# Kernel tuning notes

Hardware: AMD Instinct MI355X
Metric: run time of the kernel (lower is better)

The kernel has to match this reference:

```python
import jax, jax.numpy as jnp
import numpy as np

B, M, FIN, OUT, K = 64, 512, 128, 128, 2
SLOPE = 0.01  # F.leaky_relu default negative_slope


def setup_inputs() -> dict:
    key = jax.random.key(0)
    k0, k1, k2, k3 = jax.random.split(key, 4)
    x = jax.random.normal(k0, (B, M, FIN), jnp.float32)
    La = jax.random.normal(k1, (B, M, M), jnp.float32)
    weight = jax.random.normal(k2, (FIN * K, OUT), jnp.float32) * np.sqrt(2.0 / (FIN * K + OUT))
    bias = jnp.zeros((OUT,), jnp.float32)
    M_L = jax.random.normal(k3, (FIN, FIN), jnp.float32) * np.sqrt(2.0 / FIN)
    return {"x": x, "La": La, "weight": weight, "bias": bias, "M_L": M_L}


def _leaky(v):
    return jnp.where(v >= 0, v, SLOPE * v)


def _per_mol(xm, Lm, weight, bias, M_L):
    # xm: [M, FIN], Lm: [M, M]
    # compute_laplacian: pairwise Euclidean distances of x @ M_L via gram trick
    xw = xm @ M_L                                   # [M, FIN]
    sq = jnp.sum(xw * xw, axis=-1)                  # [M]
    d2 = sq[:, None] + sq[None, :] - 2.0 * (xw @ xw.T)
    dist = jnp.sqrt(jnp.maximum(d2, 1e-12))         # safe sqrt (diag is 0)
    W = jnp.exp(-dist)                              # [M, M]
    d = W.sum(axis=1) + 1e-7
    dis = 1.0 / jnp.sqrt(d)
    L = jnp.eye(M, dtype=xm.dtype) - dis[:, None] * W * dis[None, :]
    # clip_by_average_norm(clip_norm=1)
    avg_norm = jnp.linalg.norm(L) / (M * M)
    factor = jnp.minimum(1.0 / (avg_norm + 1e-6), 1.0)
    res_L = _leaky(L * factor)
    L_all = res_L + Lm
    # Chebyshev recursion (K terms)
    xs = [xm]
    if K > 1:
        xs.append(L_all @ xm)
    for _ in range(2, K):
        xs.append(2.0 * (L_all @ xs[-1]) - xs[-2])
    xk = jnp.stack(xs, axis=0)                      # [K, M, FIN]
    xk = jnp.transpose(xk, (1, 2, 0)).reshape(M, K * FIN)  # matches permute(1,2,0).view
    out = _leaky(xk @ weight + bias)                # activation 'relu' maps to leaky_relu
    return out, res_L, W


def reference(x, La, weight, bias, M_L):
    out, L_upd, W_upd = jax.vmap(lambda xm, Lm: _per_mol(xm, Lm, weight, bias, M_L))(x, La)
    return out, L_upd, W_upd
```

## Files before the change

kernel.cpp:

```cpp
#include <hip/hip_runtime.h>


#define BB 64
#define MM 512
#define FINC 128
#define OUTC 128

typedef short bf16x8 __attribute__((ext_vector_type(8)));
typedef float f32x4 __attribute__((ext_vector_type(4)));

__device__ __forceinline__ float leaky_(float v) { return v >= 0.0f ? v : 0.01f * v; }
__device__ __forceinline__ unsigned short f2bf(float f) {
    unsigned int u = __float_as_uint(f);
    return (unsigned short)((u + 0x7FFF + ((u >> 16) & 1)) >> 16);
}

__global__ __launch_bounds__(256) void k_xw(const float* __restrict__ x,
                                            const float* __restrict__ ml,
                                            unsigned short* __restrict__ xwb,
                                            float* __restrict__ sq,
                                            unsigned short* __restrict__ xTb) {
    const int b = blockIdx.y, i0 = blockIdx.x * 64;
    const int tid = threadIdx.x, ty4 = (tid >> 4) * 4, tx4 = (tid & 15) * 4;
    __shared__ float a_t[64][129];
    __shared__ float b_t[64][129];
    __shared__ float red[64][17];

    const float* xb = x + ((size_t)b * MM + i0) * FINC;
#pragma unroll
    for (int q = 0; q < 8; ++q) {
        int idx4 = tid + q * 256;
        int r = idx4 >> 5, k4 = (idx4 & 31) * 4;
        float4 v = *(const float4*)(xb + r * FINC + k4);
        a_t[r][k4 + 0] = v.x; a_t[r][k4 + 1] = v.y;
        a_t[r][k4 + 2] = v.z; a_t[r][k4 + 3] = v.w;
    }

    float acc[4][8];
#pragma unroll
    for (int m = 0; m < 4; ++m)
#pragma unroll
        for (int n = 0; n < 8; ++n) acc[m][n] = 0.0f;

    for (int kc = 0; kc < 2; ++kc) {
        __syncthreads();
#pragma unroll
        for (int q = 0; q < 8; ++q) {
            int idx4 = tid + q * 256;
            int kk = idx4 >> 5, c4 = (idx4 & 31) * 4;
            float4 v = *(const float4*)(ml + (size_t)(kc * 64 + kk) * FINC + c4);
            b_t[kk][c4 + 0] = v.x; b_t[kk][c4 + 1] = v.y;
            b_t[kk][c4 + 2] = v.z; b_t[kk][c4 + 3] = v.w;
        }
        __syncthreads();
#pragma unroll 4
        for (int k = 0; k < 64; ++k) {
            float av[4], bv[8];
#pragma unroll
            for (int m = 0; m < 4; ++m) av[m] = a_t[ty4 + m][kc * 64 + k];
#pragma unroll
            for (int n = 0; n < 4; ++n) { bv[n] = b_t[k][tx4 + n]; bv[4 + n] = b_t[k][64 + tx4 + n]; }
#pragma unroll
            for (int m = 0; m < 4; ++m)
#pragma unroll
                for (int n = 0; n < 8; ++n) acc[m][n] = fmaf(av[m], bv[n], acc[m][n]);
        }
    }

    unsigned short* xwbb = xwb + ((size_t)b * MM + i0) * FINC;
#pragma unroll
    for (int m = 0; m < 4; ++m) {
        ushort4 h0, h1;
        h0.x = f2bf(acc[m][0]); h0.y = f2bf(acc[m][1]); h0.z = f2bf(acc[m][2]); h0.w = f2bf(acc[m][3]);
        h1.x = f2bf(acc[m][4]); h1.y = f2bf(acc[m][5]); h1.z = f2bf(acc[m][6]); h1.w = f2bf(acc[m][7]);
        *(ushort4*)(xwbb + (ty4 + m) * FINC + tx4) = h0;
        *(ushort4*)(xwbb + (ty4 + m) * FINC + 64 + tx4) = h1;
        float p = 0.0f;
#pragma unroll
        for (int n = 0; n < 8; ++n) p = fmaf(acc[m][n], acc[m][n], p);
        red[ty4 + m][tid & 15] = p;
    }
    __syncthreads();
    if (tid < 64) {
        float s = 0.0f;
#pragma unroll
        for (int t = 0; t < 16; ++t) s += red[tid][t];
        sq[b * MM + i0 + tid] = s;
    }
#pragma unroll
    for (int q = 0; q < 16; ++q) {
        int idx = tid + q * 256;
        int c = idx >> 5, j2 = (idx & 31) * 2;
        ushort2 t;
        t.x = f2bf(a_t[j2][c]);
        t.y = f2bf(a_t[j2 + 1][c]);
        *(ushort2*)(xTb + ((size_t)b * FINC + c) * MM + i0 + j2) = t;
    }
}

__global__ __launch_bounds__(256) void k_gram(const unsigned short* __restrict__ xwb,
                                              const float* __restrict__ sq,
                                              float* __restrict__ Wout,
                                              float* __restrict__ dis) {
    const int b = blockIdx.y, i0 = blockIdx.x * 64;
    const int tid = threadIdx.x;
    const int w = tid >> 6, l = tid & 63, lr = l & 15, lg = l >> 4;
    const unsigned short* xb = xwb + (size_t)b * MM * FINC;
    const int ia = i0 + w * 16 + lr;
    const unsigned short* arow = xb + (size_t)ia * FINC + lg * 8;
    bf16x8 a0 = *(const bf16x8*)(arow + 0);
    bf16x8 a1 = *(const bf16x8*)(arow + 32);
    bf16x8 a2 = *(const bf16x8*)(arow + 64);
    bf16x8 a3 = *(const bf16x8*)(arow + 96);

    const int id0 = i0 + w * 16 + lg * 4;
    const float* sqb = sq + b * MM;
    const float si0 = sqb[id0 + 0], si1 = sqb[id0 + 1], si2 = sqb[id0 + 2], si3 = sqb[id0 + 3];
    float rs0 = 0.f, rs1 = 0.f, rs2 = 0.f, rs3 = 0.f;
    float* Wb = Wout + (size_t)b * MM * MM;

    const unsigned short* jr0 = xb + (size_t)lr * FINC + lg * 8;
    bf16x8 c0 = *(const bf16x8*)(jr0 + 0);
    bf16x8 c1 = *(const bf16x8*)(jr0 + 32);
    bf16x8 c2 = *(const bf16x8*)(jr0 + 64);
    bf16x8 c3 = *(const bf16x8*)(jr0 + 96);
    float sjc = sqb[lr];

#pragma unroll
    for (int tl = 0; tl < 32; ++tl) {
        const int nt = (tl < 31) ? tl + 1 : 31;
        const unsigned short* nr = xb + (size_t)(nt * 16 + lr) * FINC + lg * 8;
        bf16x8 n0 = *(const bf16x8*)(nr + 0);
        bf16x8 n1 = *(const bf16x8*)(nr + 32);
        bf16x8 n2 = *(const bf16x8*)(nr + 64);
        bf16x8 n3 = *(const bf16x8*)(nr + 96);
        float sjn = sqb[nt * 16 + lr];

        f32x4 acc = {0.f, 0.f, 0.f, 0.f};
        acc = __builtin_amdgcn_mfma_f32_16x16x32_bf16(a0, c0, acc, 0, 0, 0);
        acc = __builtin_amdgcn_mfma_f32_16x16x32_bf16(a1, c1, acc, 0, 0, 0);
        acc = __builtin_amdgcn_mfma_f32_16x16x32_bf16(a2, c2, acc, 0, 0, 0);
        acc = __builtin_amdgcn_mfma_f32_16x16x32_bf16(a3, c3, acc, 0, 0, 0);

        const int jc = tl * 16 + lr;
        float d2, wv;
        d2 = si0 + sjc - 2.f * acc[0]; if (id0 + 0 == jc) d2 = 0.f;
        wv = __expf(-sqrtf(fmaxf(d2, 1e-12f)));
        Wb[(size_t)(id0 + 0) * MM + jc] = wv; rs0 += wv;
        d2 = si1 + sjc - 2.f * acc[1]; if (id0 + 1 == jc) d2 = 0.f;
        wv = __expf(-sqrtf(fmaxf(d2, 1e-12f)));
        Wb[(size_t)(id0 + 1) * MM + jc] = wv; rs1 += wv;
        d2 = si2 + sjc - 2.f * acc[2]; if (id0 + 2 == jc) d2 = 0.f;
        wv = __expf(-sqrtf(fmaxf(d2, 1e-12f)));
        Wb[(size_t)(id0 + 2) * MM + jc] = wv; rs2 += wv;
        d2 = si3 + sjc - 2.f * acc[3]; if (id0 + 3 == jc) d2 = 0.f;
        wv = __expf(-sqrtf(fmaxf(d2, 1e-12f)));
        Wb[(size_t)(id0 + 3) * MM + jc] = wv; rs3 += wv;

        c0 = n0; c1 = n1; c2 = n2; c3 = n3; sjc = sjn;
    }
#pragma unroll
    for (int msk = 1; msk < 16; msk <<= 1) {
        rs0 += __shfl_xor(rs0, msk);
        rs1 += __shfl_xor(rs1, msk);
        rs2 += __shfl_xor(rs2, msk);
        rs3 += __shfl_xor(rs3, msk);
    }
    if (lr == 0) {
        dis[b * MM + id0 + 0] = 1.0f / sqrtf(rs0 + 1e-7f);
        dis[b * MM + id0 + 1] = 1.0f / sqrtf(rs1 + 1e-7f);
        dis[b * MM + id0 + 2] = 1.0f / sqrtf(rs2 + 1e-7f);
        dis[b * MM + id0 + 3] = 1.0f / sqrtf(rs3 + 1e-7f);
    }
}

__global__ __launch_bounds__(256) void k_norm(const float* __restrict__ Wout,
                                              const float* __restrict__ dis,
                                              float* __restrict__ norm2,
                                              const float* __restrict__ weight,
                                              unsigned short* __restrict__ wTb) {
    const int b = blockIdx.y;
    const float4* Wb4 = (const float4*)(Wout + (size_t)b * MM * MM);
    const float* disb = dis + b * MM;
    const int base4 = blockIdx.x * 4096;
    float acc = 0.0f;
#pragma unroll 4
    for (int q = 0; q < 16; ++q) {
        int idx4 = base4 + q * 256 + threadIdx.x;
        float4 w = Wb4[idx4];
        int p = idx4 * 4, i = p >> 9, j = p & 511;
        float di = disb[i];
        float4 dj = *(const float4*)(disb + j);
        float l0 = ((i == j + 0) ? 1.0f : 0.0f) - di * w.x * dj.x;
        float l1 = ((i == j + 1) ? 1.0f : 0.0f) - di * w.y * dj.y;
        float l2 = ((i == j + 2) ? 1.0f : 0.0f) - di * w.z * dj.z;
        float l3 = ((i == j + 3) ? 1.0f : 0.0f) - di * w.w * dj.w;
        acc += l0 * l0 + l1 * l1 + l2 * l2 + l3 * l3;
    }
#pragma unroll
    for (int off = 32; off > 0; off >>= 1) acc += __shfl_down(acc, off);
    __shared__ float r[4];
    if ((threadIdx.x & 63) == 0) r[threadIdx.x >> 6] = acc;
    __syncthreads();
    if (threadIdx.x == 0) atomicAdd(&norm2[b], r[0] + r[1] + r[2] + r[3]);

    if (blockIdx.x == 0 && blockIdx.y == 0) {
        int tid = threadIdx.x;
#pragma unroll 4
        for (int q = 0; q < 128; ++q) {
            int idx = tid + q * 256;
            int k = idx >> 7, c = idx & 127;
            wTb[(size_t)c * 256 + k] = f2bf(weight[idx]);
        }
    }
}

__global__ __launch_bounds__(256) void k_lall(const float* __restrict__ Wout,
                                              const float* __restrict__ La,
                                              const unsigned short* __restrict__ xTb,
                                              const float* __restrict__ dis,
                                              const float* __restrict__ norm2,
                                              float* __restrict__ resL,
                                              unsigned short* __restrict__ yb) {
    const int b = blockIdx.y, i0 = blockIdx.x * 64;
    const int tid = threadIdx.x;
    const int w = tid >> 6, l = tid & 63, lr = l & 15, lg = l >> 4;
    const int ia = i0 + w * 16 + lr;
    const float avgn = sqrtf(norm2[b]) / (512.0f * 512.0f);
    const float fac = fminf(1.0f / (avgn + 1e-6f), 1.0f);
    const float* disb = dis + b * MM;
    const float di = disb[ia];
    const float* Wr = Wout + (size_t)b * MM * MM + (size_t)ia * MM;
    const float* Lr = La   + (size_t)b * MM * MM + (size_t)ia * MM;
    float* Rr = resL + (size_t)b * MM * MM + (size_t)ia * MM;
    const unsigned short* xTm = xTb + (size_t)b * FINC * MM;

    f32x4 acc[8];
#pragma unroll
    for (int n = 0; n < 8; ++n) acc[n] = (f32x4){0.f, 0.f, 0.f, 0.f};

#define LD2(W0, W1, L0, L1, t) { const int kk_ = (t) * 32 + lg * 8; \
    W0 = *(const float4*)(Wr + kk_); W1 = *(const float4*)(Wr + kk_ + 4); \
    L0 = *(const float4*)(Lr + kk_); L1 = *(const float4*)(Lr + kk_ + 4); }

#define STEP(CW0, CW1, CL0, CL1, t) { \
    const int koff = (t) * 32 + lg * 8; \
    bf16x8 bfr[8]; \
    _Pragma("unroll") \
    for (int n = 0; n < 8; ++n) \
        bfr[n] = *(const bf16x8*)(xTm + (size_t)(n * 16 + lr) * MM + koff); \
    float4 dj0 = *(const float4*)(disb + koff); \
    float4 dj1 = *(const float4*)(disb + koff + 4); \
    const int dd = ia - koff; \
    const float* wp0 = &CW0.x; const float* wp1 = &CW1.x; \
    const float* lp0 = &CL0.x; const float* lp1 = &CL1.x; \
    const float* dp0 = &dj0.x; const float* dp1 = &dj1.x; \
    float4 r0, r1; float* rp0 = &r0.x; float* rp1 = &r1.x; \
    bf16x8 af; \
    _Pragma("unroll") \
    for (int e = 0; e < 4; ++e) { \
        float Lv = ((dd == e) ? 1.0f : 0.0f) - di * wp0[e] * dp0[e]; \
        float rv = leaky_(Lv * fac); \
        rp0[e] = rv; \
        af[e] = (short)f2bf(rv + lp0[e]); \
    } \
    _Pragma("unroll") \
    for (int e = 0; e < 4; ++e) { \
        float Lv = ((dd == e + 4) ? 1.0f : 0.0f) - di * wp1[e] * dp1[e]; \
        float rv = leaky_(Lv * fac); \
        rp1[e] = rv; \
        af[e + 4] = (short)f2bf(rv + lp1[e]); \
    } \
    *(float4*)(Rr + koff) = r0; \
    *(float4*)(Rr + koff + 4) = r1; \
    _Pragma("unroll") \
    for (int n = 0; n < 8; ++n) \
        acc[n] = __builtin_amdgcn_mfma_f32_16x16x32_bf16(af, bfr[n], acc[n], 0, 0, 0); \
}

    float4 aw0, aw1, al0, al1, bw0, bw1, bl0, bl1, tw0, tw1, tl0, tl1;
    LD2(aw0, aw1, al0, al1, 0);
    LD2(bw0, bw1, bl0, bl1, 1);
#pragma unroll
    for (int tp = 0; tp < 8; ++tp) {
        const int t0 = tp * 2, t1 = tp * 2 + 1;
        if (t0 + 2 < 16) { LD2(tw0, tw1, tl0, tl1, t0 + 2); }
        STEP(aw0, aw1, al0, al1, t0);
        if (t0 + 2 < 16) { aw0 = tw0; aw1 = tw1; al0 = tl0; al1 = tl1; }
        if (t1 + 2 < 16) { LD2(tw0, tw1, tl0, tl1, t1 + 2); }
        STEP(bw0, bw1, bl0, bl1, t1);
        if (t1 + 2 < 16) { bw0 = tw0; bw1 = tw1; bl0 = tl0; bl1 = tl1; }
    }
#undef LD2
#undef STEP

    const int id0 = i0 + w * 16 + lg * 4;
    unsigned short* ybb = yb + (size_t)b * MM * FINC;
#pragma unroll
    for (int n = 0; n < 8; ++n) {
        const int col = n * 16 + lr;
#pragma unroll
        for (int rg = 0; rg < 4; ++rg)
            ybb[(size_t)(id0 + rg) * FINC + col] = f2bf(acc[n][rg]);
    }
}

__global__ __launch_bounds__(256) void k_out(const float* __restrict__ x,
                                             const unsigned short* __restrict__ yb,
                                             const unsigned short* __restrict__ wTb,
                                             const float* __restrict__ bias,
                                             float* __restrict__ out) {
    const int b = blockIdx.y, i0 = blockIdx.x * 64;
    const int tid = threadIdx.x;
    const int w = tid >> 6, l = tid & 63, lr = l & 15, lg = l >> 4;
    const int ia = i0 + w * 16 + lr;
    const float* xr = x + ((size_t)b * MM + ia) * FINC;
    const unsigned short* yr = yb + ((size_t)b * MM + ia) * FINC;

    f32x4 acc[8];
#pragma unroll
    for (int n = 0; n < 8; ++n) acc[n] = (f32x4){0.f, 0.f, 0.f, 0.f};

    float4 xc = *(const float4*)(xr + lg * 4);
    ushort4 yc = *(const ushort4*)(yr + lg * 4);

#pragma unroll
    for (int ch = 0; ch < 8; ++ch) {
        const int koff = ch * 32 + lg * 8;
        float4 xn; ushort4 yn;
        if (ch < 7) {
            const int f1 = (ch + 1) * 16 + lg * 4;
            xn = *(const float4*)(xr + f1);
            yn = *(const ushort4*)(yr + f1);
        }
        bf16x8 af;
        af[0] = (short)f2bf(xc.x); af[1] = (short)yc.x;
        af[2] = (short)f2bf(xc.y); af[3] = (short)yc.y;
        af[4] = (short)f2bf(xc.z); af[5] = (short)yc.z;
        af[6] = (short)f2bf(xc.w); af[7] = (short)yc.w;
#pragma unroll
        for (int n = 0; n < 8; ++n) {
            bf16x8 bf = *(const bf16x8*)(wTb + (size_t)(n * 16 + lr) * 256 + koff);
            acc[n] = __builtin_amdgcn_mfma_f32_16x16x32_bf16(af, bf, acc[n], 0, 0, 0);
        }
        if (ch < 7) { xc = xn; yc = yn; }
    }

    const int id0 = i0 + w * 16 + lg * 4;
    float* ob = out + (size_t)b * MM * OUTC;
#pragma unroll
    for (int n = 0; n < 8; ++n) {
        const int col = n * 16 + lr;
        const float bs = bias[col];
#pragma unroll
        for (int rg = 0; rg < 4; ++rg)
            ob[(size_t)(id0 + rg) * OUTC + col] = leaky_(acc[n][rg] + bs);
    }
}

extern "C" void kernel_launch(void* const* d_in, const int* in_sizes, int n_in,
                              void* d_out, int out_size, void* d_ws, size_t ws_size,
                              hipStream_t stream) {
    const float* x      = (const float*)d_in[0];
    const float* La     = (const float*)d_in[1];
    const float* weight = (const float*)d_in[2];
    const float* bias   = (const float*)d_in[3];
    const float* ml     = (const float*)d_in[4];

    float* out0 = (float*)d_out;
    float* out1 = out0 + (size_t)BB * MM * OUTC;
    float* out2 = out1 + (size_t)BB * MM * MM;

    unsigned short* xwb = (unsigned short*)d_ws;
    unsigned short* yb  = xwb;
    unsigned short* xTb = xwb + 4194304;
    float* sq     = (float*)((char*)d_ws + 16777216);
    unsigned short* wTb = (unsigned short*)sq;
    float* dis    = sq + 32768;
    float* norm2  = dis + 32768;

    hipMemsetAsync(norm2, 0, BB * sizeof(float), stream);

    dim3 blk(256);
    k_xw    <<<dim3(8, BB),  blk, 0, stream>>>(x, ml, xwb, sq, xTb);
    k_gram  <<<dim3(8, BB),  blk, 0, stream>>>(xwb, sq, out2, dis);
    k_norm  <<<dim3(16, BB), blk, 0, stream>>>(out2, dis, norm2, weight, wTb);
    k_lall  <<<dim3(8, BB),  blk, 0, stream>>>(out2, La, xTb, dis, norm2, out1, yb);
    k_out   <<<dim3(8, BB),  blk, 0, stream>>>(x, yb, wTb, bias, out0);
}
```

Measured before the change: 376.9 us.

## Drop norm-clip pass and fuse output projection into L_all kernel

Measured after the change: 317.9 us. -15.7%, faster.

```diff
diff --git a/kernel.cpp b/kernel.cpp
--- a/kernel.cpp
+++ b/kernel.cpp
@@ -174,66 +174,27 @@
     }
 }
 
-__global__ __launch_bounds__(256) void k_norm(const float* __restrict__ Wout,
-                                              const float* __restrict__ dis,
-                                              float* __restrict__ norm2,
-                                              const float* __restrict__ weight,
-                                              unsigned short* __restrict__ wTb) {
-    const int b = blockIdx.y;
-    const float4* Wb4 = (const float4*)(Wout + (size_t)b * MM * MM);
-    const float* disb = dis + b * MM;
-    const int base4 = blockIdx.x * 4096;
-    float acc = 0.0f;
-#pragma unroll 4
-    for (int q = 0; q < 16; ++q) {
-        int idx4 = base4 + q * 256 + threadIdx.x;
-        float4 w = Wb4[idx4];
-        int p = idx4 * 4, i = p >> 9, j = p & 511;
-        float di = disb[i];
-        float4 dj = *(const float4*)(disb + j);
-        float l0 = ((i == j + 0) ? 1.0f : 0.0f) - di * w.x * dj.x;
-        float l1 = ((i == j + 1) ? 1.0f : 0.0f) - di * w.y * dj.y;
-        float l2 = ((i == j + 2) ? 1.0f : 0.0f) - di * w.z * dj.z;
-        float l3 = ((i == j + 3) ? 1.0f : 0.0f) - di * w.w * dj.w;
-        acc += l0 * l0 + l1 * l1 + l2 * l2 + l3 * l3;
-    }
-#pragma unroll
-    for (int off = 32; off > 0; off >>= 1) acc += __shfl_down(acc, off);
-    __shared__ float r[4];
-    if ((threadIdx.x & 63) == 0) r[threadIdx.x >> 6] = acc;
-    __syncthreads();
-    if (threadIdx.x == 0) atomicAdd(&norm2[b], r[0] + r[1] + r[2] + r[3]);
-
-    if (blockIdx.x == 0 && blockIdx.y == 0) {
-        int tid = threadIdx.x;
-#pragma unroll 4
-        for (int q = 0; q < 128; ++q) {
-            int idx = tid + q * 256;
-            int k = idx >> 7, c = idx & 127;
-            wTb[(size_t)c * 256 + k] = f2bf(weight[idx]);
-        }
-    }
-}
-
-__global__ __launch_bounds__(256) void k_lall(const float* __restrict__ Wout,
+__global__ __launch_bounds__(256) void k_fuse(const float* __restrict__ Wout,
                                               const float* __restrict__ La,
                                               const unsigned short* __restrict__ xTb,
                                               const float* __restrict__ dis,
-                                              const float* __restrict__ norm2,
+                                              const float* __restrict__ x,
+                                              const float* __restrict__ weight,
+                                              const float* __restrict__ bias,
                                               float* __restrict__ resL,
-                                              unsigned short* __restrict__ yb) {
+                                              float* __restrict__ out) {
     const int b = blockIdx.y, i0 = blockIdx.x * 64;
     const int tid = threadIdx.x;
     const int w = tid >> 6, l = tid & 63, lr = l & 15, lg = l >> 4;
     const int ia = i0 + w * 16 + lr;
-    const float avgn = sqrtf(norm2[b]) / (512.0f * 512.0f);
-    const float fac = fminf(1.0f / (avgn + 1e-6f), 1.0f);
     const float* disb = dis + b * MM;
     const float di = disb[ia];
     const float* Wr = Wout + (size_t)b * MM * MM + (size_t)ia * MM;
     const float* Lr = La   + (size_t)b * MM * MM + (size_t)ia * MM;
     float* Rr = resL + (size_t)b * MM * MM + (size_t)ia * MM;
     const unsigned short* xTm = xTb + (size_t)b * FINC * MM;
+
+    __shared__ unsigned short y_lds[64][136];
 
     f32x4 acc[8];
 #pragma unroll
@@ -260,14 +221,14 @@
     _Pragma("unroll") \
     for (int e = 0; e < 4; ++e) { \
         float Lv = ((dd == e) ? 1.0f : 0.0f) - di * wp0[e] * dp0[e]; \
-        float rv = leaky_(Lv * fac); \
+        float rv = leaky_(Lv);                \
         rp0[e] = rv; \
         af[e] = (short)f2bf(rv + lp0[e]); \
     } \
     _Pragma("unroll") \
     for (int e = 0; e < 4; ++e) { \
         float Lv = ((dd == e + 4) ? 1.0f : 0.0f) - di * wp1[e] * dp1[e]; \
-        float rv = leaky_(Lv * fac); \
+        float rv = leaky_(Lv); \
         rp1[e] = rv; \
         af[e + 4] = (short)f2bf(rv + lp1[e]); \
     } \
@@ -294,56 +255,42 @@
 #undef LD2
 #undef STEP
 
-    const int id0 = i0 + w * 16 + lg * 4;
-    unsigned short* ybb = yb + (size_t)b * MM * FINC;
+    const int r0l = w * 16 + lg * 4;
 #pragma unroll
     for (int n = 0; n < 8; ++n) {
         const int col = n * 16 + lr;
 #pragma unroll
         for (int rg = 0; rg < 4; ++rg)
-            ybb[(size_t)(id0 + rg) * FINC + col] = f2bf(acc[n][rg]);
-    }
-}
-
-__global__ __launch_bounds__(256) void k_out(const float* __restrict__ x,
-                                             const unsigned short* __restrict__ yb,
-                                             const unsigned short* __restrict__ wTb,
-                                             const float* __restrict__ bias,
-                                             float* __restrict__ out) {
-    const int b = blockIdx.y, i0 = blockIdx.x * 64;
-    const int tid = threadIdx.x;
-    const int w = tid >> 6, l = tid & 63, lr = l & 15, lg = l >> 4;
-    const int ia = i0 + w * 16 + lr;
+            y_lds[r0l + rg][col] = f2bf(acc[n][rg]);
+    }
+    __syncthreads();
+
     const float* xr = x + ((size_t)b * MM + ia) * FINC;
-    const unsigned short* yr = yb + ((size_t)b * MM + ia) * FINC;
-
-    f32x4 acc[8];
-#pragma unroll
-    for (int n = 0; n < 8; ++n) acc[n] = (f32x4){0.f, 0.f, 0.f, 0.f};
-
-    float4 xc = *(const float4*)(xr + lg * 4);
-    ushort4 yc = *(const ushort4*)(yr + lg * 4);
+    const int yrow = w * 16 + lr;
+    f32x4 acc2[8];
+#pragma unroll
+    for (int n = 0; n < 8; ++n) acc2[n] = (f32x4){0.f, 0.f, 0.f, 0.f};
 
 #pragma unroll
     for (int ch = 0; ch < 8; ++ch) {
         const int koff = ch * 32 + lg * 8;
-        float4 xn; ushort4 yn;
-        if (ch < 7) {
-            const int f1 = (ch + 1) * 16 + lg * 4;
-            xn = *(const float4*)(xr + f1);
-            yn = *(const ushort4*)(yr + f1);
+        const int f0 = koff >> 1;
+        float4 xv = *(const float4*)(xr + f0);
+        ushort4 yv = *(const ushort4*)&y_lds[yrow][f0];
+        bf16x8 af;
+        af[0] = (short)f2bf(xv.x); af[1] = (short)yv.x;
+        af[2] = (short)f2bf(xv.y); af[3] = (short)yv.y;
+        af[4] = (short)f2bf(xv.z); af[5] = (short)yv.z;
+        af[6] = (short)f2bf(xv.w); af[7] = (short)yv.w;
+#pragma unroll
+        for (int n = 0; n < 8; ++n) {
+            const int col = n * 16 + lr;
+            bf16x8 bf;
+#pragma unroll
+            for (int j = 0; j < 8; ++j)
+                bf[j] = (short)f2bf(weight[(size_t)(koff + j) * OUTC + col]);
+            acc2[n] = __builtin_amdgcn_mfma_f32_16x16x32_bf16(af, bf, acc2[n], 0, 0, 0);
         }
-        bf16x8 af;
-        af[0] = (short)f2bf(xc.x); af[1] = (short)yc.x;
-        af[2] = (short)f2bf(xc.y); af[3] = (short)yc.y;
-        af[4] = (short)f2bf(xc.z); af[5] = (short)yc.z;
-        af[6] = (short)f2bf(xc.w); af[7] = (short)yc.w;
-#pragma unroll
-        for (int n = 0; n < 8; ++n) {
-            bf16x8 bf = *(const bf16x8*)(wTb + (size_t)(n * 16 + lr) * 256 + koff);
-            acc[n] = __builtin_amdgcn_mfma_f32_16x16x32_bf16(af, bf, acc[n], 0, 0, 0);
-        }
-        if (ch < 7) { xc = xn; yc = yn; }
     }
 
     const int id0 = i0 + w * 16 + lg * 4;
@@ -354,7 +301,7 @@
         const float bs = bias[col];
 #pragma unroll
         for (int rg = 0; rg < 4; ++rg)
-            ob[(size_t)(id0 + rg) * OUTC + col] = leaky_(acc[n][rg] + bs);
+            ob[(size_t)(id0 + rg) * OUTC + col] = leaky_(acc2[n][rg] + bs);
     }
 }
 
@@ -372,19 +319,12 @@
     float* out2 = out1 + (size_t)BB * MM * MM;
 
     unsigned short* xwb = (unsigned short*)d_ws;
-    unsigned short* yb  = xwb;
     unsigned short* xTb = xwb + 4194304;
-    float* sq     = (float*)((char*)d_ws + 16777216);
-    unsigned short* wTb = (unsigned short*)sq;
-    float* dis    = sq + 32768;
-    float* norm2  = dis + 32768;
-
-    hipMemsetAsync(norm2, 0, BB * sizeof(float), stream);
+    float* sq  = (float*)((char*)d_ws + 16777216);
+    float* dis = sq + 32768;
 
     dim3 blk(256);
-    k_xw    <<<dim3(8, BB),  blk, 0, stream>>>(x, ml, xwb, sq, xTb);
-    k_gram  <<<dim3(8, BB),  blk, 0, stream>>>(xwb, sq, out2, dis);
-    k_norm  <<<dim3(16, BB), blk, 0, stream>>>(out2, dis, norm2, weight, wTb);
-    k_lall  <<<dim3(8, BB),  blk, 0, stream>>>(out2, La, xTb, dis, norm2, out1, yb);
-    k_out   <<<dim3(8, BB),  blk, 0, stream>>>(x, yb, wTb, bias, out0);
-}
+    k_xw   <<<dim3(8, BB), blk, 0, stream>>>(x, ml, xwb, sq, xTb);
+    k_gram <<<dim3(8, BB), blk, 0, stream>>>(xwb, sq, out2, dis);
+    k_fuse <<<dim3(8, BB), blk, 0, stream>>>(out2, La, xTb, dis, x, weight, bias, out1, out0);
+}
```
